# Kernel optimization log

Measured on AMD Instinct MI355X. Metric: run time of the kernel, lower is better.

The kernel has to match this reference:

```python
import jax, jax.numpy as jnp
import numpy as np

N_NODES = 21
N_ACTIONS = 256
NODE_FEAT = 128


def _gcn_norm(edge_index, n):
    # Dense normalized adjacency mirroring PyG gcn_norm with add_self_loops=True.
    row, col = edge_index[0], edge_index[1]
    A = jnp.zeros((n, n), dtype=jnp.float32).at[row, col].add(1.0)
    A = A + jnp.eye(n, dtype=jnp.float32)  # self loops appended with weight 1
    deg = A.sum(axis=0)                    # scatter-add of edge weights by col
    dinv = jnp.where(deg > 0, 1.0 / jnp.sqrt(deg), 0.0)
    # out[row] += dinv[row] * dinv[col] * x[col]  ->  A_norm = D^-1/2 A D^-1/2
    return dinv[:, None] * A * dinv[None, :]


def setup_inputs() -> dict:
    key = jax.random.key(0)
    ks = jax.random.split(key, 12)
    B = 65536
    state = jax.random.normal(ks[0], (B, N_NODES, NODE_FEAT), dtype=jnp.float32)
    edge_index = jax.random.randint(ks[1], (2, 128), 0, N_NODES, dtype=jnp.int32)

    def lin(k, fan_in, fan_out):
        s = 1.0 / np.sqrt(fan_in)
        kw, kb = jax.random.split(k)
        W = jax.random.uniform(kw, (fan_in, fan_out), jnp.float32, -s, s)
        b = jax.random.uniform(kb, (fan_out,), jnp.float32, -s, s)
        return W, b

    W1, b1 = lin(ks[2], NODE_FEAT, 21)
    W2, b2 = lin(ks[3], 21, 21)
    Wf1, bf1 = lin(ks[4], 441, 512)
    Wf2, bf2 = lin(ks[5], 512, 512)
    Wf3, bf3 = lin(ks[6], 512, N_ACTIONS)
    return {"state": state, "edge_index": edge_index,
            "W1": W1, "b1": b1, "W2": W2, "b2": b2,
            "Wf1": Wf1, "bf1": bf1, "Wf2": Wf2, "bf2": bf2,
            "Wf3": Wf3, "bf3": bf3}


def reference(state, edge_index, W1, b1, W2, b2, Wf1, bf1, Wf2, bf2, Wf3, bf3):
    A = _gcn_norm(edge_index, N_NODES)                      # [21, 21]
    # GCNConv 1: A_norm @ (X W1) + b1   (no nonlinearity between GCN layers)
    h = jnp.einsum('bnf,fh->bnh', state, W1)                # [B, 21, 21]
    h = jnp.einsum('ij,bjh->bih', A, h) + b1
    # GCNConv 2
    h = jnp.einsum('bnf,fh->bnh', h, W2)
    h = jnp.einsum('ij,bjh->bih', A, h) + b2                # [B, 21, 21]
    v = h.reshape(h.shape[0], -1)[0]                        # x.view(B,-1)[0] -> [441]
    x = jax.nn.relu(v @ Wf1 + bf1)
    x = jax.nn.relu(x @ Wf2 + bf2)
    x = jax.nn.relu(x @ Wf3 + bf3)                          # [n_actions]
    return x
```

## Files before the change

### kernel.cpp

```cpp
#include <hip/hip_runtime.h>
#include <math.h>

#define N_NODES 21
#define NODE_FEAT 128
#define N_ACTIONS 256
#define APAD 28
#define W1PAD 132

#define WS_ACC1 0
#define WS_ACC2 512
#define WS_ACC3 1024

__device__ unsigned g_arrive[64 * 16];
__device__ unsigned g_go;
__device__ unsigned g_cnt;

__device__ __forceinline__ float agent_load(const float* p) {
    return __hip_atomic_load(p, __ATOMIC_RELAXED, __HIP_MEMORY_SCOPE_AGENT);
}
__device__ __forceinline__ void agent_store(float* p, float v) {
    __hip_atomic_store(p, v, __ATOMIC_RELAXED, __HIP_MEMORY_SCOPE_AGENT);
}
__device__ __forceinline__ unsigned flag_load(const unsigned* p) {
    return __hip_atomic_load(p, __ATOMIC_RELAXED, __HIP_MEMORY_SCOPE_AGENT);
}
__device__ __forceinline__ void flag_store(unsigned* p, unsigned v) {
    __hip_atomic_store(p, v, __ATOMIC_RELAXED, __HIP_MEMORY_SCOPE_AGENT);
}
__device__ __forceinline__ float agent_fadd(float* p, float v) {
    return __hip_atomic_fetch_add(p, v, __ATOMIC_RELAXED, __HIP_MEMORY_SCOPE_AGENT);
}

__device__ __forceinline__ void lds_barrier() {
    asm volatile("s_waitcnt lgkmcnt(0)\n\ts_barrier" ::: "memory");
}

__device__ __forceinline__ void grid_barrier(int blk, unsigned base, unsigned phase) {
    const unsigned target = base + phase;
    __syncthreads();
    if (blk == 0) {
        if (threadIdx.x > 0 && threadIdx.x < 64) {
            for (;;) {
                unsigned f = flag_load(&g_arrive[threadIdx.x * 16]);
                if ((int)(f - target) >= 0) break;
                __builtin_amdgcn_s_sleep(1);
            }
        }
        if (threadIdx.x == 0) flag_store(&g_go, target);
    } else {
        if (threadIdx.x == 0) {
            flag_store(&g_arrive[blk * 16], target);
            for (;;) {
                unsigned f = flag_load(&g_go);
                if ((int)(f - target) >= 0) break;
                __builtin_amdgcn_s_sleep(1);
            }
        }
    }
    __syncthreads();
}

__global__ __launch_bounds__(512) void fused_kernel(
    const float* __restrict__ state,
    const int*   __restrict__ edge_index,
    const float* __restrict__ W1,
    const float* __restrict__ b1,
    const float* __restrict__ W2,
    const float* __restrict__ b2,
    const float* __restrict__ Wf1,
    const float* __restrict__ bf1,
    const float* __restrict__ Wf2,
    const float* __restrict__ bf2,
    const float* __restrict__ Wf3,
    const float* __restrict__ bf3,
    float* __restrict__ ws,
    float* __restrict__ out)
{
    const int b = blockIdx.x;
    const int t = threadIdx.x;

    const unsigned bbase = flag_load(&g_go);
    const unsigned cbase = flag_load(&g_cnt);

    __shared__ float sA[21 * APAD];
    __shared__ float sX[21 * W1PAD];
    __shared__ float sW1T[21 * W1PAD];
    __shared__ float sW2T[21 * APAD];
    __shared__ float sT[21 * APAD];
    __shared__ float sG[21 * APAD];
    __shared__ float sv[441];
    __shared__ float sdeg[21];
    __shared__ float sb1[21], sb2[21];
    __shared__ float x1s[8], x2s[8];
    __shared__ unsigned sflag;

    for (int i = t; i < 21 * APAD; i += 512) {
        sA[i] = 0.0f; sW2T[i] = 0.0f; sT[i] = 0.0f; sG[i] = 0.0f;
    }
    if (t < 21) { sdeg[t] = 1.0f; sb1[t] = b1[t]; sb2[t] = b2[t]; }
    {
        const float4* src4 = (const float4*)state;
        for (int i = t; i < 672; i += 512) {
            int n = i >> 5, fc = i & 31;
            ((float4*)&sX[n * W1PAD])[fc] = src4[i];
        }
    }
    for (int i = t; i < 2688; i += 512) {
        int f = i / 21, k = i - f * 21;
        sW1T[k * W1PAD + f] = W1[i];
    }
    for (int i = t; i < 441; i += 512) {
        int f = i / 21, k = i - f * 21;
        sW2T[k * APAD + f] = W2[i];
    }
    int er = 0, ec = 0;
    if (t < 128) { er = edge_index[t]; ec = edge_index[128 + t]; }

    float wf1v[7];
    if (b < 63) {
        #pragma unroll
        for (int i = 0; i < 7; ++i) wf1v[i] = Wf1[(size_t)(7 * b + i) * 512 + t];
    }
    float wf2v[8];
    #pragma unroll
    for (int i = 0; i < 8; ++i) wf2v[i] = Wf2[(size_t)(8 * b + i) * 512 + t];
    float wf3v[8];
    if (t < 256) {
        #pragma unroll
        for (int i = 0; i < 8; ++i) wf3v[i] = Wf3[(size_t)(8 * b + i) * 256 + t];
    }
    const float rbf1 = (t < 8) ? bf1[8 * b + t] : 0.0f;
    const float rbf2 = (t < 8) ? bf2[8 * b + t] : 0.0f;
    const float rbf3 = bf3[t & 255];

    if (b == 0) {
        agent_store(&ws[WS_ACC1 + t], 0.0f);
        agent_store(&ws[WS_ACC2 + t], 0.0f);
        if (t < 256) agent_store(&ws[WS_ACC3 + t], 0.0f);
    }

    if (b == 0) __syncthreads(); else lds_barrier();
    if (b == 0 && t == 0) flag_store(&g_go, bbase + 1);

    if (t < 128) {
        atomicAdd(&sA[er * APAD + ec], 1.0f);
        atomicAdd(&sdeg[ec], 1.0f);
    }
    if (t < 21) atomicAdd(&sA[t * APAD + t], 1.0f);
    if (t < 441) {
        int n = t / 21, k = t - n * 21;
        const float4* x4 = (const float4*)&sX[n * W1PAD];
        const float4* w4 = (const float4*)&sW1T[k * W1PAD];
        float s = 0.0f;
        #pragma unroll
        for (int fc = 0; fc < 32; ++fc) {
            float4 a = x4[fc], ww = w4[fc];
            s += a.x * ww.x; s += a.y * ww.y; s += a.z * ww.z; s += a.w * ww.w;
        }
        sT[k * APAD + n] = s;
    }
    lds_barrier();

    if (t < 441) {
        int r = t / 21, c = t - r * 21;
        float dr = 1.0f / sqrtf(sdeg[r]);
        float dc = 1.0f / sqrtf(sdeg[c]);
        sA[r * APAD + c] = dr * sA[r * APAD + c] * dc;
    }
    lds_barrier();

    if (t < 441) {
        int r = t / 21, k = t - r * 21;
        const float4* a4 = (const float4*)&sA[r * APAD];
        const float4* h4 = (const float4*)&sT[k * APAD];
        float s = sb1[k];
        #pragma unroll
        for (int jc = 0; jc < 6; ++jc) {
            float4 a = a4[jc], h = h4[jc];
            s += a.x * h.x; s += a.y * h.y; s += a.z * h.z; s += a.w * h.w;
        }
        sG[r * APAD + k] = s;
    }
    lds_barrier();

    if (t < 441) {
        int n = t / 21, k = t - n * 21;
        const float4* g4 = (const float4*)&sG[n * APAD];
        const float4* w4 = (const float4*)&sW2T[k * APAD];
        float s = 0.0f;
        #pragma unroll
        for (int jc = 0; jc < 6; ++jc) {
            float4 g = g4[jc], ww = w4[jc];
            s += g.x * ww.x; s += g.y * ww.y; s += g.z * ww.z; s += g.w * ww.w;
        }
        sT[k * APAD + n] = s;
    }
    lds_barrier();

    if (t < 441) {
        int r = t / 21, k = t - r * 21;
        const float4* a4 = (const float4*)&sA[r * APAD];
        const float4* h4 = (const float4*)&sT[k * APAD];
        float s = sb2[k];
        #pragma unroll
        for (int jc = 0; jc < 6; ++jc) {
            float4 a = a4[jc], h = h4[jc];
            s += a.x * h.x; s += a.y * h.y; s += a.z * h.z; s += a.w * h.w;
        }
        sv[t] = s;
    }
    lds_barrier();

    if (t == 0) {
        while ((int)(flag_load(&g_go) - (bbase + 1)) < 0)
            __builtin_amdgcn_s_sleep(1);
    }
    __syncthreads();

    if (b < 63) {
        float s = 0.0f;
        #pragma unroll
        for (int r = 0; r < 7; ++r) s += sv[7 * b + r] * wf1v[r];
        agent_fadd(&ws[WS_ACC1 + t], s);
    }

    grid_barrier(b, bbase, 2);

    if (t < 8) x1s[t] = fmaxf(agent_load(&ws[WS_ACC1 + 8 * b + t]) + rbf1, 0.0f);
    lds_barrier();
    {
        float s = 0.0f;
        #pragma unroll
        for (int j = 0; j < 8; ++j) s += x1s[j] * wf2v[j];
        agent_fadd(&ws[WS_ACC2 + t], s);
    }

    grid_barrier(b, bbase, 3);

    if (t < 8) x2s[t] = fmaxf(agent_load(&ws[WS_ACC2 + 8 * b + t]) + rbf2, 0.0f);
    lds_barrier();
    if (t < 256) {
        float s = 0.0f;
        #pragma unroll
        for (int j = 0; j < 8; ++j) s += x2s[j] * wf3v[j];
        agent_fadd(&ws[WS_ACC3 + t], s);
    }

    __syncthreads();
    if (t == 0) {
        unsigned prev = __hip_atomic_fetch_add(&g_cnt, 1u, __ATOMIC_RELAXED,
                                               __HIP_MEMORY_SCOPE_AGENT);
        sflag = (prev == cbase + 63u) ? 1u : 0u;
    }
    __syncthreads();
    if (sflag && t < 256) {
        float a = agent_load(&ws[WS_ACC3 + t]) + rbf3;
        out[t] = fmaxf(a, 0.0f);
    }
}

extern "C" void kernel_launch(void* const* d_in, const int* in_sizes, int n_in,
                              void* d_out, int out_size, void* d_ws, size_t ws_size,
                              hipStream_t stream)
{
    const float* state      = (const float*)d_in[0];
    const int*   edge_index = (const int*)  d_in[1];
    const float* W1  = (const float*)d_in[2];
    const float* b1  = (const float*)d_in[3];
    const float* W2  = (const float*)d_in[4];
    const float* b2  = (const float*)d_in[5];
    const float* Wf1 = (const float*)d_in[6];
    const float* bf1 = (const float*)d_in[7];
    const float* Wf2 = (const float*)d_in[8];
    const float* bf2 = (const float*)d_in[9];
    const float* Wf3 = (const float*)d_in[10];
    const float* bf3 = (const float*)d_in[11];

    float* ws  = (float*)d_ws;
    float* out = (float*)d_out;

    fused_kernel<<<64, 512, 0, stream>>>(state, edge_index, W1, b1, W2, b2,
                                         Wf1, bf1, Wf2, bf2, Wf3, bf3, ws, out);
}
```

Before: 17.39 us.

## Replace float atomics with per-block partial buffers reduced by wavefront shuffles

The fused kernel no longer accumulates each dense layer with device-scope float atomic adds into a shared accumulator. Each block now writes its partial sums to its own slot in a workspace buffer, and after the grid barrier every wavefront reduces its 64 partials with xor shuffles. This also removes the zero-initialisation phase and its extra go-flag wait. The last block sums the per-block layer-3 partials itself. The old atomic version is kept as a fallback for when the workspace is too small; the new path adds more global traffic and depends on the workspace size.

```diff
diff --git a/kernel.cpp b/kernel.cpp
--- a/kernel.cpp
+++ b/kernel.cpp
@@ -3,9 +3,13 @@
 
 #define N_NODES 21
 #define NODE_FEAT 128
-#define N_ACTIONS 256
 #define APAD 28
 #define W1PAD 132
+
+#define WS_P1 0
+#define WS_P2 (512 * 64)
+#define WS_P3 (2 * 512 * 64)
+#define WS_NEED_BYTES ((2 * 512 * 64 + 64 * 256) * 4)
 
 #define WS_ACC1 0
 #define WS_ACC2 512
@@ -61,20 +65,210 @@
 }
 
 __global__ __launch_bounds__(512) void fused_kernel(
-    const float* __restrict__ state,
-    const int*   __restrict__ edge_index,
-    const float* __restrict__ W1,
-    const float* __restrict__ b1,
-    const float* __restrict__ W2,
-    const float* __restrict__ b2,
-    const float* __restrict__ Wf1,
-    const float* __restrict__ bf1,
-    const float* __restrict__ Wf2,
-    const float* __restrict__ bf2,
-    const float* __restrict__ Wf3,
-    const float* __restrict__ bf3,
-    float* __restrict__ ws,
-    float* __restrict__ out)
+    const float* __restrict__ state, const int* __restrict__ edge_index,
+    const float* __restrict__ W1, const float* __restrict__ b1,
+    const float* __restrict__ W2, const float* __restrict__ b2,
+    const float* __restrict__ Wf1, const float* __restrict__ bf1,
+    const float* __restrict__ Wf2, const float* __restrict__ bf2,
+    const float* __restrict__ Wf3, const float* __restrict__ bf3,
+    float* __restrict__ ws, float* __restrict__ out)
+{
+    const int b = blockIdx.x;
+    const int t = threadIdx.x;
+    const int r6 = t >> 6, j6 = t & 63;
+
+    const unsigned bbase = flag_load(&g_go);
+    const unsigned cbase = flag_load(&g_cnt);
+
+    __shared__ float sA[21 * APAD];
+    __shared__ float sX[21 * W1PAD];
+    __shared__ float sW1T[21 * W1PAD];
+    __shared__ float sW2T[21 * APAD];
+    __shared__ float sT[21 * APAD];
+    __shared__ float sG[21 * APAD];
+    __shared__ float sv[441];
+    __shared__ float sdeg[21];
+    __shared__ float sb1[21], sb2[21];
+    __shared__ float x1s[8], x2s[8];
+    __shared__ float xs[512];
+    __shared__ unsigned sflag;
+
+    for (int i = t; i < 21 * APAD; i += 512) {
+        sA[i] = 0.0f; sW2T[i] = 0.0f; sT[i] = 0.0f; sG[i] = 0.0f;
+    }
+    if (t < 21) { sdeg[t] = 1.0f; sb1[t] = b1[t]; sb2[t] = b2[t]; }
+    {
+        const float4* src4 = (const float4*)state;
+        for (int i = t; i < 672; i += 512) {
+            int n = i >> 5, fc = i & 31;
+            ((float4*)&sX[n * W1PAD])[fc] = src4[i];
+        }
+    }
+    for (int i = t; i < 2688; i += 512) {
+        int f = i / 21, k = i - f * 21;
+        sW1T[k * W1PAD + f] = W1[i];
+    }
+    for (int i = t; i < 441; i += 512) {
+        int f = i / 21, k = i - f * 21;
+        sW2T[k * APAD + f] = W2[i];
+    }
+    int er = 0, ec = 0;
+    if (t < 128) { er = edge_index[t]; ec = edge_index[128 + t]; }
+
+    float wf1v[7];
+    if (b < 63) {
+        #pragma unroll
+        for (int i = 0; i < 7; ++i) wf1v[i] = Wf1[(size_t)(7 * b + i) * 512 + t];
+    }
+    float wf2v[8];
+    #pragma unroll
+    for (int i = 0; i < 8; ++i) wf2v[i] = Wf2[(size_t)(8 * b + i) * 512 + t];
+    float wf3v[8];
+    if (t < 256) {
+        #pragma unroll
+        for (int i = 0; i < 8; ++i) wf3v[i] = Wf3[(size_t)(8 * b + i) * 256 + t];
+    }
+    const float rbf1w = bf1[8 * b + r6];
+    const float rbf2w = bf2[8 * b + r6];
+    const float rbf3  = bf3[t & 255];
+
+    lds_barrier();
+
+    if (t < 128) {
+        atomicAdd(&sA[er * APAD + ec], 1.0f);
+        atomicAdd(&sdeg[ec], 1.0f);
+    }
+    if (t < 21) atomicAdd(&sA[t * APAD + t], 1.0f);
+    if (t < 441) {
+        int n = t / 21, k = t - n * 21;
+        const float4* x4 = (const float4*)&sX[n * W1PAD];
+        const float4* w4 = (const float4*)&sW1T[k * W1PAD];
+        float s = 0.0f;
+        #pragma unroll
+        for (int fc = 0; fc < 32; ++fc) {
+            float4 a = x4[fc], ww = w4[fc];
+            s += a.x * ww.x; s += a.y * ww.y; s += a.z * ww.z; s += a.w * ww.w;
+        }
+        sT[k * APAD + n] = s;
+    }
+    lds_barrier();
+
+    if (t < 441) {
+        int r = t / 21, c = t - r * 21;
+        float dr = 1.0f / sqrtf(sdeg[r]);
+        float dc = 1.0f / sqrtf(sdeg[c]);
+        sA[r * APAD + c] = dr * sA[r * APAD + c] * dc;
+    }
+    lds_barrier();
+
+    if (t < 441) {
+        int r = t / 21, k = t - r * 21;
+        const float4* a4 = (const float4*)&sA[r * APAD];
+        const float4* h4 = (const float4*)&sT[k * APAD];
+        float s = sb1[k];
+        #pragma unroll
+        for (int jc = 0; jc < 6; ++jc) {
+            float4 a = a4[jc], h = h4[jc];
+            s += a.x * h.x; s += a.y * h.y; s += a.z * h.z; s += a.w * h.w;
+        }
+        sG[r * APAD + k] = s;
+    }
+    lds_barrier();
+
+    if (t < 441) {
+        int n = t / 21, k = t - n * 21;
+        const float4* g4 = (const float4*)&sG[n * APAD];
+        const float4* w4 = (const float4*)&sW2T[k * APAD];
+        float s = 0.0f;
+        #pragma unroll
+        for (int jc = 0; jc < 6; ++jc) {
+            float4 g = g4[jc], ww = w4[jc];
+            s += g.x * ww.x; s += g.y * ww.y; s += g.z * ww.z; s += g.w * ww.w;
+        }
+        sT[k * APAD + n] = s;
+    }
+    lds_barrier();
+
+    if (t < 441) {
+        int r = t / 21, k = t - r * 21;
+        const float4* a4 = (const float4*)&sA[r * APAD];
+        const float4* h4 = (const float4*)&sT[k * APAD];
+        float s = sb2[k];
+        #pragma unroll
+        for (int jc = 0; jc < 6; ++jc) {
+            float4 a = a4[jc], h = h4[jc];
+            s += a.x * h.x; s += a.y * h.y; s += a.z * h.z; s += a.w * h.w;
+        }
+        sv[t] = s;
+    }
+    lds_barrier();
+
+    if (b < 63) {
+        float s = 0.0f;
+        #pragma unroll
+        for (int r = 0; r < 7; ++r) s += sv[7 * b + r] * wf1v[r];
+        agent_store(&ws[WS_P1 + t * 64 + b], s);
+    }
+
+    grid_barrier(b, bbase, 1);
+
+    {
+        float p = (j6 < 63) ? agent_load(&ws[WS_P1 + (8 * b + r6) * 64 + j6]) : 0.0f;
+        #pragma unroll
+        for (int m = 32; m; m >>= 1) p += __shfl_xor(p, m, 64);
+        if (j6 == 0) x1s[r6] = fmaxf(p + rbf1w, 0.0f);
+    }
+    lds_barrier();
+    {
+        float s = 0.0f;
+        #pragma unroll
+        for (int j = 0; j < 8; ++j) s += x1s[j] * wf2v[j];
+        agent_store(&ws[WS_P2 + t * 64 + b], s);
+    }
+
+    grid_barrier(b, bbase, 2);
+
+    {
+        float p = agent_load(&ws[WS_P2 + (8 * b + r6) * 64 + j6]);
+        #pragma unroll
+        for (int m = 32; m; m >>= 1) p += __shfl_xor(p, m, 64);
+        if (j6 == 0) x2s[r6] = fmaxf(p + rbf2w, 0.0f);
+    }
+    lds_barrier();
+    if (t < 256) {
+        float s = 0.0f;
+        #pragma unroll
+        for (int j = 0; j < 8; ++j) s += x2s[j] * wf3v[j];
+        agent_store(&ws[WS_P3 + b * 256 + t], s);
+    }
+
+    __syncthreads();
+    if (t == 0) {
+        unsigned prev = __hip_atomic_fetch_add(&g_cnt, 1u, __ATOMIC_RELAXED,
+                                               __HIP_MEMORY_SCOPE_AGENT);
+        sflag = (prev == cbase + 63u) ? 1u : 0u;
+    }
+    __syncthreads();
+    if (sflag) {
+        const int c = t & 255, h = t >> 8;
+        float s = 0.0f;
+        #pragma unroll
+        for (int j = 0; j < 32; ++j)
+            s += agent_load(&ws[WS_P3 + (h * 32 + j) * 256 + c]);
+        xs[t] = s;
+    }
+    lds_barrier();
+    if (sflag && t < 256) out[t] = fmaxf(xs[t] + xs[t + 256] + rbf3, 0.0f);
+}
+
+__global__ __launch_bounds__(512) void fused_kernel_atomic(
+    const float* __restrict__ state, const int* __restrict__ edge_index,
+    const float* __restrict__ W1, const float* __restrict__ b1,
+    const float* __restrict__ W2, const float* __restrict__ b2,
+    const float* __restrict__ Wf1, const float* __restrict__ bf1,
+    const float* __restrict__ Wf2, const float* __restrict__ bf2,
+    const float* __restrict__ Wf3, const float* __restrict__ bf3,
+    float* __restrict__ ws, float* __restrict__ out)
 {
     const int b = blockIdx.x;
     const int t = threadIdx.x;
@@ -138,7 +332,6 @@
         agent_store(&ws[WS_ACC2 + t], 0.0f);
         if (t < 256) agent_store(&ws[WS_ACC3 + t], 0.0f);
     }
-
     if (b == 0) __syncthreads(); else lds_barrier();
     if (b == 0 && t == 0) flag_store(&g_go, bbase + 1);
 
@@ -160,7 +353,6 @@
         sT[k * APAD + n] = s;
     }
     lds_barrier();
-
     if (t < 441) {
         int r = t / 21, c = t - r * 21;
         float dr = 1.0f / sqrtf(sdeg[r]);
@@ -168,7 +360,6 @@
         sA[r * APAD + c] = dr * sA[r * APAD + c] * dc;
     }
     lds_barrier();
-
     if (t < 441) {
         int r = t / 21, k = t - r * 21;
         const float4* a4 = (const float4*)&sA[r * APAD];
@@ -182,7 +373,6 @@
         sG[r * APAD + k] = s;
     }
     lds_barrier();
-
     if (t < 441) {
         int n = t / 21, k = t - n * 21;
         const float4* g4 = (const float4*)&sG[n * APAD];
@@ -196,7 +386,6 @@
         sT[k * APAD + n] = s;
     }
     lds_barrier();
-
     if (t < 441) {
         int r = t / 21, k = t - r * 21;
         const float4* a4 = (const float4*)&sA[r * APAD];
@@ -223,7 +412,6 @@
         for (int r = 0; r < 7; ++r) s += sv[7 * b + r] * wf1v[r];
         agent_fadd(&ws[WS_ACC1 + t], s);
     }
-
     grid_barrier(b, bbase, 2);
 
     if (t < 8) x1s[t] = fmaxf(agent_load(&ws[WS_ACC1 + 8 * b + t]) + rbf1, 0.0f);
@@ -234,7 +422,6 @@
         for (int j = 0; j < 8; ++j) s += x1s[j] * wf2v[j];
         agent_fadd(&ws[WS_ACC2 + t], s);
     }
-
     grid_barrier(b, bbase, 3);
 
     if (t < 8) x2s[t] = fmaxf(agent_load(&ws[WS_ACC2 + 8 * b + t]) + rbf2, 0.0f);
@@ -279,6 +466,11 @@
     float* ws  = (float*)d_ws;
     float* out = (float*)d_out;
 
-    fused_kernel<<<64, 512, 0, stream>>>(state, edge_index, W1, b1, W2, b2,
-                                         Wf1, bf1, Wf2, bf2, Wf3, bf3, ws, out);
-}
+    if (ws_size >= (size_t)WS_NEED_BYTES) {
+        fused_kernel<<<64, 512, 0, stream>>>(state, edge_index, W1, b1, W2, b2,
+                                             Wf1, bf1, Wf2, bf2, Wf3, bf3, ws, out);
+    } else {
+        fused_kernel_atomic<<<64, 512, 0, stream>>>(state, edge_index, W1, b1, W2, b2,
+                                                    Wf1, bf1, Wf2, bf2, Wf3, bf3, ws, out);
+    }
+}
```

Result: slower. 19.01 us (+9.4%).

## Repartition FC layers across block subsets with larger per-block row chunks

Applied to the files above, without the earlier changes.

Reassigns the three fully connected layers so that FC1 runs on blocks 0-20 with 21 rows each, FC2 on blocks 21-52 with 16 rows each, and FC3 on blocks 0-31 with 16 rows each. The old scheme spread every layer over all 64 blocks in chunks of 7 or 8 rows. The aim is fewer global atomic adds per accumulator and less contention at each grid barrier, plus overlap of the weight prefetch across different blocks. In exchange each active block does more serial work and holds more registers, and some blocks sit idle in each phase.

```diff
diff --git a/kernel.cpp b/kernel.cpp
--- a/kernel.cpp
+++ b/kernel.cpp
@@ -3,7 +3,6 @@
 
 #define N_NODES 21
 #define NODE_FEAT 128
-#define N_ACTIONS 256
 #define APAD 28
 #define W1PAD 132
 
@@ -82,6 +81,10 @@
     const unsigned bbase = flag_load(&g_go);
     const unsigned cbase = flag_load(&g_cnt);
 
+    const bool do_fc1 = (b < 21);
+    const bool do_fc2 = (b >= 21 && b < 53);
+    const bool do_fc3 = (b < 32);
+
     __shared__ float sA[21 * APAD];
     __shared__ float sX[21 * W1PAD];
     __shared__ float sW1T[21 * W1PAD];
@@ -91,7 +94,7 @@
     __shared__ float sv[441];
     __shared__ float sdeg[21];
     __shared__ float sb1[21], sb2[21];
-    __shared__ float x1s[8], x2s[8];
+    __shared__ float x1s[16], x2s[16];
     __shared__ unsigned sflag;
 
     for (int i = t; i < 21 * APAD; i += 512) {
@@ -116,21 +119,27 @@
     int er = 0, ec = 0;
     if (t < 128) { er = edge_index[t]; ec = edge_index[128 + t]; }
 
-    float wf1v[7];
-    if (b < 63) {
-        #pragma unroll
-        for (int i = 0; i < 7; ++i) wf1v[i] = Wf1[(size_t)(7 * b + i) * 512 + t];
-    }
-    float wf2v[8];
-    #pragma unroll
-    for (int i = 0; i < 8; ++i) wf2v[i] = Wf2[(size_t)(8 * b + i) * 512 + t];
-    float wf3v[8];
-    if (t < 256) {
-        #pragma unroll
-        for (int i = 0; i < 8; ++i) wf3v[i] = Wf3[(size_t)(8 * b + i) * 256 + t];
-    }
-    const float rbf1 = (t < 8) ? bf1[8 * b + t] : 0.0f;
-    const float rbf2 = (t < 8) ? bf2[8 * b + t] : 0.0f;
+    float wf1v[21];
+    if (do_fc1) {
+        #pragma unroll
+        for (int i = 0; i < 21; ++i) wf1v[i] = Wf1[(size_t)(21 * b + i) * 512 + t];
+    }
+    float wf2v[16];
+    float rbf1 = 0.0f;
+    if (do_fc2) {
+        #pragma unroll
+        for (int i = 0; i < 16; ++i) wf2v[i] = Wf2[(size_t)(16 * (b - 21) + i) * 512 + t];
+        if (t < 16) rbf1 = bf1[16 * (b - 21) + t];
+    }
+    float wf3v[16];
+    float rbf2 = 0.0f;
+    if (do_fc3) {
+        if (t < 256) {
+            #pragma unroll
+            for (int i = 0; i < 16; ++i) wf3v[i] = Wf3[(size_t)(16 * b + i) * 256 + t];
+        }
+        if (t < 16) rbf2 = bf2[16 * b + t];
+    }
     const float rbf3 = bf3[t & 255];
 
     if (b == 0) {
@@ -217,33 +226,37 @@
     }
     __syncthreads();
 
-    if (b < 63) {
-        float s = 0.0f;
-        #pragma unroll
-        for (int r = 0; r < 7; ++r) s += sv[7 * b + r] * wf1v[r];
+    if (do_fc1) {
+        float s = 0.0f;
+        #pragma unroll
+        for (int r = 0; r < 21; ++r) s += sv[21 * b + r] * wf1v[r];
         agent_fadd(&ws[WS_ACC1 + t], s);
     }
 
     grid_barrier(b, bbase, 2);
 
-    if (t < 8) x1s[t] = fmaxf(agent_load(&ws[WS_ACC1 + 8 * b + t]) + rbf1, 0.0f);
-    lds_barrier();
-    {
-        float s = 0.0f;
-        #pragma unroll
-        for (int j = 0; j < 8; ++j) s += x1s[j] * wf2v[j];
+    if (do_fc2) {
+        if (t < 16)
+            x1s[t] = fmaxf(agent_load(&ws[WS_ACC1 + 16 * (b - 21) + t]) + rbf1, 0.0f);
+        lds_barrier();
+        float s = 0.0f;
+        #pragma unroll
+        for (int j = 0; j < 16; ++j) s += x1s[j] * wf2v[j];
         agent_fadd(&ws[WS_ACC2 + t], s);
     }
 
     grid_barrier(b, bbase, 3);
 
-    if (t < 8) x2s[t] = fmaxf(agent_load(&ws[WS_ACC2 + 8 * b + t]) + rbf2, 0.0f);
-    lds_barrier();
-    if (t < 256) {
-        float s = 0.0f;
-        #pragma unroll
-        for (int j = 0; j < 8; ++j) s += x2s[j] * wf3v[j];
-        agent_fadd(&ws[WS_ACC3 + t], s);
+    if (do_fc3) {
+        if (t < 16)
+            x2s[t] = fmaxf(agent_load(&ws[WS_ACC2 + 16 * b + t]) + rbf2, 0.0f);
+        lds_barrier();
+        if (t < 256) {
+            float s = 0.0f;
+            #pragma unroll
+            for (int j = 0; j < 16; ++j) s += x2s[j] * wf3v[j];
+            agent_fadd(&ws[WS_ACC3 + t], s);
+        }
     }
 
     __syncthreads();
```

Result: faster. 16.38 us (-5.8%).
